# Optimization experiments

Measured on AMD Instinct MI355X. Metric: run time of the kernel, lower is better.

## Reference

```python
import jax, jax.numpy as jnp
import numpy as np

# Quantization / threshold constants (from init_kwargs)
AQI, AQF = 8, 8      # activation fixed-point: int/frac bits
NQI, NQF = 2, 8      # nonlinearity output fixed-point
TH_X = 0.1           # delta threshold on input
TH_H = 0.1           # delta threshold on hidden state


def _round_ste(x):
    # straight-through round (GradPreserveRoundTensor in the original util)
    return x + jax.lax.stop_gradient(jnp.round(x) - x)


def quantize(x, qi, qf):
    # util.quantize_tensor with quantize=1: fake-quantize to Q(qi).(qf) fixed point
    power = jnp.asarray(2.0 ** qf, x.dtype)
    clip_val = 2.0 ** (qi + qf - 1)
    return jnp.clip(_round_ste(x * power), -clip_val, clip_val - 1) / power


def setup_inputs() -> dict:
    key = jax.random.key(0)
    k0, k1, k2, k3, k4 = jax.random.split(key, 5)
    T, B, I, H = 512, 64, 512, 1024
    G = 4 * H
    return {
        "x": jax.random.normal(k0, (T, B, I), jnp.float32),
        "weight_ih": jax.random.normal(k1, (G, I), jnp.float32) / np.sqrt(I).astype(np.float32),
        "weight_hh": jax.random.normal(k2, (G, H), jnp.float32) / np.sqrt(H).astype(np.float32),
        "bias_ih": jax.random.normal(k3, (G,), jnp.float32) * 0.1,
        "bias_hh": jax.random.normal(k4, (G,), jnp.float32) * 0.1,
    }


def reference(x, weight_ih, weight_hh, bias_ih, bias_hh):
    T, B, I = x.shape
    H = weight_hh.shape[1]
    dt = x.dtype

    th_x_q = quantize(jnp.asarray(TH_X, dt), AQI, AQF)  # quantized threshold for delta mask
    th_h_q = quantize(jnp.asarray(TH_H, dt), AQI, AQF)

    xs = quantize(x, AQI, AQF)  # inputs quantized once up front

    # initial state (initialize_state with state=None)
    x_prev0 = jnp.zeros((B, I), dt)           # Q(zeros) == zeros
    h0 = jnp.zeros((B, H), dt)
    hp0 = jnp.zeros((B, H), dt)
    c0 = jnp.zeros((B, H), dt)
    m0 = jnp.zeros((B, 4 * H), dt) + bias_ih + bias_hh  # biases folded into m once
    reg0 = jnp.zeros((), dt)

    w_ih_t = weight_ih.T  # [I, 4H]
    w_hh_t = weight_hh.T  # [H, 4H]

    def step(carry, x_t):
        x_prev, h, h_prev, c, m, reg = carry
        dx = x_t - x_prev
        dh = h - h_prev
        dxa = jnp.abs(dx)
        dha = jnp.abs(dh)
        dx = jnp.where(dxa < th_x_q, jnp.asarray(0, dt), dx)   # masked_fill with quantized th
        dh = jnp.where(dha < th_h_q, jnp.asarray(0, dt), dh)
        x_prev = jnp.where(dxa >= TH_X, x_t, x_prev)           # state update with raw th (as in source)
        h_prev = jnp.where(dha >= TH_H, h, h_prev)
        reg = reg + jnp.sum(jnp.abs(dh))                       # l1 norm of masked delta_h

        m = dx @ w_ih_t + dh @ w_hh_t + m                      # delta-GEMM accumulated into m
        pre = quantize(m, AQI, AQF)
        p_i, p_f, p_g, p_o = jnp.split(pre, 4, axis=1)
        g_i = quantize(jax.nn.sigmoid(p_i), NQI, NQF)
        g_f = quantize(jax.nn.sigmoid(p_f), NQI, NQF)
        g_o = quantize(jax.nn.sigmoid(p_o), NQI, NQF)
        g_g = quantize(jnp.tanh(p_g), NQI, NQF)

        c_new = c * g_f + g_i * g_g
        q_c = quantize(c_new, AQI, AQF)
        c_tanh = quantize(jnp.tanh(q_c), NQI, NQF)
        h_new = quantize(g_o * c_tanh, AQI, AQF)
        return (x_prev, h_new, h_prev, q_c, m, reg), h_new

    (x_prev, h, h_prev, c, m, reg), out = jax.lax.scan(
        step, (x_prev0, h0, hp0, c0, m0, reg0), xs)

    # x_prev_out is padded to [B, max(I, H)] (zeros beyond input_size)
    x_prev_out = jnp.zeros((B, max(I, H)), dt).at[:, :I].set(x_prev)
    # state tensors stacked over layers (num_layers=1)
    state = (x_prev_out[None], h[None], h_prev[None], c[None], m[None])
    return (out, *state, reg.reshape(1))
```

## Files before the change

### kernel.cpp

```cpp
#include <hip/hip_runtime.h>
#include <hip/hip_fp16.h>
#include <stdint.h>

typedef unsigned short ushort_t;
typedef unsigned int uint_t;
typedef unsigned long long ull_t;
typedef _Float16 half8 __attribute__((ext_vector_type(8)));
typedef float f32x4 __attribute__((ext_vector_type(4)));

#define TSTEPS 512
#define BATCH  64
#define ISZ    512
#define HSZ    1024
#define GSZ    4096
#define NB     256
#define NTH    1024
#define DHFRAG 65536

static constexpr size_t OFF_XPREV = (size_t)TSTEPS * BATCH * HSZ;
static constexpr size_t OFF_H     = OFF_XPREV + (size_t)BATCH * 1024;
static constexpr size_t OFF_HP    = OFF_H  + (size_t)BATCH * HSZ;
static constexpr size_t OFF_C     = OFF_HP + (size_t)BATCH * HSZ;
static constexpr size_t OFF_M     = OFF_C  + (size_t)BATCH * HSZ;
static constexpr size_t OFF_REG   = OFF_M  + (size_t)BATCH * GSZ;

#define TH_RAW 0.1f
#define TH_QNT 0.1015625f

__device__ __forceinline__ float qA(float x) {
  float v = rintf(x * 256.0f);
  v = fminf(fmaxf(v, -32768.0f), 32767.0f);
  return v * 0.00390625f;
}
__device__ __forceinline__ float qN(float x) {
  float v = rintf(x * 256.0f);
  v = fminf(fmaxf(v, -512.0f), 511.0f);
  return v * 0.00390625f;
}
__device__ __forceinline__ float sigm(float x) { return 1.0f / (1.0f + expf(-x)); }

__global__ __launch_bounds__(256) void xscan_kernel(const float* __restrict__ x,
                                                    __half* __restrict__ dx16,
                                                    float* __restrict__ out_xprev) {
  const int gid = blockIdx.x * blockDim.x + threadIdx.x;
  float xp = 0.0f;
  #pragma unroll 8
  for (int t = 0; t < TSTEPS; t++) {
    float xq = qA(x[(size_t)t * (BATCH * ISZ) + gid]);
    float d  = xq - xp;
    float da = fabsf(d);
    dx16[(size_t)t * (BATCH * ISZ) + gid] = __float2half((da < TH_QNT) ? 0.0f : d);
    if (da >= TH_RAW) xp = xq;
  }
  const int b = gid >> 9;
  const int i = gid & 511;
  out_xprev[(size_t)b * 1024 + i]       = xp;
  out_xprev[(size_t)b * 1024 + 512 + i] = 0.0f;
}

__device__ __forceinline__ void gbar_arrive(int* flags, int e) {
  asm volatile("s_waitcnt vmcnt(0)" ::: "memory");
  __syncthreads();
  if (threadIdx.x == 0) {
    __hip_atomic_store(&flags[blockIdx.x], e, __ATOMIC_RELAXED, __HIP_MEMORY_SCOPE_AGENT);
  }
}
__device__ __forceinline__ void gbar_wait(int* flags, int e) {
  if (threadIdx.x < 64) {
    const ull_t* f64 = (const ull_t*)flags;
    const int l = threadIdx.x;
    bool done;
    do {
      ull_t a = __hip_atomic_load(f64 + l,      __ATOMIC_RELAXED, __HIP_MEMORY_SCOPE_AGENT);
      ull_t c = __hip_atomic_load(f64 + 64 + l, __ATOMIC_RELAXED, __HIP_MEMORY_SCOPE_AGENT);
      bool ok = ((int)a >= e) & ((int)(a >> 32) >= e) &
                ((int)c >= e) & ((int)(c >> 32) >= e);
      done = __all(ok);
      if (!done) __builtin_amdgcn_s_sleep(2);
    } while (!done);
  }
  __syncthreads();
}

__global__ __launch_bounds__(NTH, 4) void scan_kernel(
    const __half* __restrict__ dx16, const float* __restrict__ w_ih,
    const float* __restrict__ w_hh, const float* __restrict__ b_ih,
    const float* __restrict__ b_hh, float* __restrict__ out,
    __half* __restrict__ dh16, float* __restrict__ partials, int* flags) {
  __shared__ __align__(16) unsigned char dxbuf[2][65536];
  __shared__ float part[4][64][16];
  __shared__ float red[256];

  const int tid  = threadIdx.x;
  const int wid  = tid >> 6;
  const int lane = tid & 63;
  const int bt   = wid >> 2;
  const int kg   = wid & 3;
  const int lr   = lane & 15;
  const int lkb  = (lane >> 4) * 16;

  const int wrow = blockIdx.x * 4 + (lr & 3) + (lr >> 2) * HSZ;
  half8 wx[4], wh[8];
  #pragma unroll
  for (int kt = 0; kt < 4; ++kt) {
    const float* p = w_ih + (size_t)wrow * ISZ + kg * 128 + kt * 32 + (lane >> 4) * 8;
    half8 v;
    #pragma unroll
    for (int e = 0; e < 8; ++e) v[e] = (_Float16)p[e];
    wx[kt] = v;
  }
  #pragma unroll
  for (int kt = 0; kt < 8; ++kt) {
    const float* p = w_hh + (size_t)wrow * HSZ + kg * 256 + kt * 32 + (lane >> 4) * 8;
    half8 v;
    #pragma unroll
    for (int e = 0; e < 8; ++e) v[e] = (_Float16)p[e];
    wh[kt] = v;
  }

  const int jj = tid & 3;
  const int cb = tid >> 2;
  const int j  = blockIdx.x * 4 + jj;
  const int g0 = j, g1 = j + HSZ, g2 = j + 2 * HSZ, g3 = j + 3 * HSZ;
  float m0 = 0.f, m1 = 0.f, m2 = 0.f, m3 = 0.f;
  float c = 0.0f, hp = 0.0f, h = 0.0f, regacc = 0.0f;
  if (tid < 256) {
    m0 = b_ih[g0] + b_hh[g0];
    m1 = b_ih[g1] + b_hh[g1];
    m2 = b_ih[g2] + b_hh[g2];
    m3 = b_ih[g3] + b_hh[g3];
  }
  const size_t dhcell2 = ((size_t)(blockIdx.x >> 1) * 64 + cb) * 2 + (blockIdx.x & 1);

  const int arow = bt * 16 + lr;
  const int akey = (arow & 7) << 4;

  const int kc0 = kg * 32 + (lane >> 4);
  const int hrow = arow;

  {
    const ull_t* __restrict__ sx = (const ull_t*)dx16;
    #pragma unroll
    for (int i = 0; i < 8; ++i) {
      ull_t v = sx[i * 1024 + tid];
      const int u = i * 1024 + tid;
      const int row = u >> 7, cc = u & 127;
      *(ull_t*)(&dxbuf[0][0] + row * 1024 + ((cc * 8) ^ ((row & 7) << 4))) = v;
    }
  }
  __syncthreads();

  int epoch = 1;

  for (int t = 0; t < TSTEPS; t++) {
    const ull_t* __restrict__ hb = (const ull_t*)(dh16 + (size_t)(t & 1) * DHFRAG);
    const unsigned char* xbase = &dxbuf[t & 1][0] + arow * 1024;

    ull_t lo[4], hi[4];
    #pragma unroll
    for (int kt = 0; kt < 4; ++kt) {
      const size_t ci = ((size_t)(kc0 + kt * 4) * 64 + hrow) * 2;
      lo[kt] = __hip_atomic_load(hb + ci,     __ATOMIC_RELAXED, __HIP_MEMORY_SCOPE_AGENT);
      hi[kt] = __hip_atomic_load(hb + ci + 1, __ATOMIC_RELAXED, __HIP_MEMORY_SCOPE_AGENT);
    }

    f32x4 acc = {0.f, 0.f, 0.f, 0.f};
    {
      #pragma unroll
      for (int kt = 0; kt < 4; ++kt) {
        const int col = kg * 256 + kt * 64 + lkb;
        union { uint4 u; half8 hv; } U;
        U.u = *(const uint4*)(xbase + (col ^ akey));
        acc = __builtin_amdgcn_mfma_f32_16x16x32_f16(U.hv, wx[kt], acc, 0, 0, 0);
      }
    }

    ull_t lo2[4], hi2[4];
    #pragma unroll
    for (int kt = 0; kt < 4; ++kt) {
      const size_t ci = ((size_t)(kc0 + (kt + 4) * 4) * 64 + hrow) * 2;
      lo2[kt] = __hip_atomic_load(hb + ci,     __ATOMIC_RELAXED, __HIP_MEMORY_SCOPE_AGENT);
      hi2[kt] = __hip_atomic_load(hb + ci + 1, __ATOMIC_RELAXED, __HIP_MEMORY_SCOPE_AGENT);
    }
    #pragma unroll
    for (int kt = 0; kt < 4; ++kt) {
      union { ull_t u[2]; half8 hv; } U;
      U.u[0] = lo[kt]; U.u[1] = hi[kt];
      acc = __builtin_amdgcn_mfma_f32_16x16x32_f16(U.hv, wh[kt], acc, 0, 0, 0);
    }
    #pragma unroll
    for (int kt = 0; kt < 4; ++kt) {
      union { ull_t u[2]; half8 hv; } U;
      U.u[0] = lo2[kt]; U.u[1] = hi2[kt];
      acc = __builtin_amdgcn_mfma_f32_16x16x32_f16(U.hv, wh[kt + 4], acc, 0, 0, 0);
    }

    #pragma unroll
    for (int r = 0; r < 4; ++r)
      part[kg][bt * 16 + (lane >> 4) * 4 + r][lr] = acc[r];
    __syncthreads();

    if (tid < 256) {
      float s0 = 0.f, s1 = 0.f, s2 = 0.f, s3 = 0.f;
      #pragma unroll
      for (int k2 = 0; k2 < 4; ++k2) {
        s0 += part[k2][cb][jj];
        s1 += part[k2][cb][4 + jj];
        s2 += part[k2][cb][8 + jj];
        s3 += part[k2][cb][12 + jj];
      }
      m0 += s0; m1 += s1; m2 += s2; m3 += s3;

      float pi = qA(m0), pf = qA(m1), pg = qA(m2), po = qA(m3);
      float gi = qN(sigm(pi));
      float gf = qN(sigm(pf));
      float gg = qN(tanhf(pg));
      float go = qN(sigm(po));
      float cn = c * gf + gi * gg;
      c = qA(cn);
      float ct = qN(tanhf(c));
      h = qA(go * ct);
      out[(size_t)t * (BATCH * HSZ) + (size_t)cb * HSZ + j] = h;

      if (t < TSTEPS - 1) {
        float d  = h - hp;
        float da = fabsf(d);
        float dm = (da < TH_QNT) ? 0.0f : d;
        if (da >= TH_RAW) hp = h;
        regacc += fabsf(dm);
        ushort_t my = __half_as_ushort(__float2half(dm));
        int v1 = __shfl((int)my, lane + 1, 64);
        int v2 = __shfl((int)my, lane + 2, 64);
        int v3 = __shfl((int)my, lane + 3, 64);
        if (jj == 0) {
          ull_t dw = (ull_t)my | ((ull_t)(ushort_t)v1 << 16) |
                     ((ull_t)(ushort_t)v2 << 32) | ((ull_t)(ushort_t)v3 << 48);
          ull_t* dhw = (ull_t*)(dh16 + (size_t)((t + 1) & 1) * DHFRAG);
          __hip_atomic_store(dhw + dhcell2, dw,
                             __ATOMIC_RELAXED, __HIP_MEMORY_SCOPE_AGENT);
        }
      }
    }

    gbar_arrive(flags, epoch);

    if (t < TSTEPS - 1) {
      const ull_t* __restrict__ sx =
          (const ull_t*)(dx16 + (size_t)(t + 1) * (BATCH * ISZ));
      unsigned char* dst = &dxbuf[(t + 1) & 1][0];
      #pragma unroll
      for (int i = 0; i < 8; ++i) {
        ull_t v = sx[i * 1024 + tid];
        const int u = i * 1024 + tid;
        const int row = u >> 7, cc = u & 127;
        *(ull_t*)(dst + row * 1024 + ((cc * 8) ^ ((row & 7) << 4))) = v;
      }
    }

    gbar_wait(flags, epoch);
    epoch++;
  }

  if (tid < 256) {
    out[OFF_H  + (size_t)cb * HSZ + j] = h;
    out[OFF_HP + (size_t)cb * HSZ + j] = hp;
    out[OFF_C  + (size_t)cb * HSZ + j] = c;
    out[OFF_M  + (size_t)cb * GSZ + g0] = m0;
    out[OFF_M  + (size_t)cb * GSZ + g1] = m1;
    out[OFF_M  + (size_t)cb * GSZ + g2] = m2;
    out[OFF_M  + (size_t)cb * GSZ + g3] = m3;
  }

  if (tid < 256) red[tid] = regacc;
  __syncthreads();
  for (int s = 128; s > 0; s >>= 1) {
    if (tid < s) red[tid] += red[tid + s];
    __syncthreads();
  }
  if (tid == 0)
    __hip_atomic_store(&partials[blockIdx.x], red[0], __ATOMIC_RELAXED, __HIP_MEMORY_SCOPE_AGENT);
  gbar_arrive(flags, epoch);
  gbar_wait(flags, epoch);
  epoch++;
  if (blockIdx.x == 0) {
    if (tid < 256)
      red[tid] = __hip_atomic_load(&partials[tid], __ATOMIC_RELAXED, __HIP_MEMORY_SCOPE_AGENT);
    __syncthreads();
    for (int s = 128; s > 0; s >>= 1) {
      if (tid < s) red[tid] += red[tid + s];
      __syncthreads();
    }
    if (tid == 0) out[OFF_REG] = red[0];
  }
}

extern "C" void kernel_launch(void* const* d_in, const int* in_sizes, int n_in,
                              void* d_out, int out_size, void* d_ws, size_t ws_size,
                              hipStream_t stream) {
  const float* x    = (const float*)d_in[0];
  const float* w_ih = (const float*)d_in[1];
  const float* w_hh = (const float*)d_in[2];
  const float* b_ih = (const float*)d_in[3];
  const float* b_hh = (const float*)d_in[4];
  float* out = (float*)d_out;

  const size_t dx_elems = (size_t)TSTEPS * BATCH * ISZ;
  __half* dx16     = (__half*)d_ws;
  __half* dh16     = dx16 + dx_elems;
  float*  partials = (float*)(dh16 + 2 * (size_t)DHFRAG);
  int*    flags    = (int*)(partials + NB);
  size_t needed = (size_t)((char*)(flags + NB) - (char*)d_ws);
  if (ws_size < needed) return;

  (void)hipMemsetAsync(dh16, 0, 2 * (size_t)DHFRAG * sizeof(__half), stream);
  (void)hipMemsetAsync(flags, 0, NB * sizeof(int), stream);
  xscan_kernel<<<128, 256, 0, stream>>>(x, dx16, out + OFF_XPREV);
  scan_kernel<<<NB, NTH, 0, stream>>>(dx16, w_ih, w_hh, b_ih, b_hh, out,
                                      dh16, partials, flags);
}
```

Baseline: 2.660 ms.

## Split batch into two groups with separate grid barriers to pipeline recurrent steps

Each timestep's batch of 64 is split into two groups of 32, each with its own dh buffer and flag set. Each block processes one group, arrives on that group's barrier, and only then waits on the other group's barrier, so barrier latency for one group can overlap compute for the other. The K dimension is split across 8 wave groups instead of 4, with a padded partial-sum buffer to cut LDS bank conflicts. Blocks are remapped to a permuted hidden-unit index. This adds a barrier and a __syncthreads per group, and the gbar_wait/arrive helpers are now called with the timestep as the epoch, so correctness depends on those helpers matching that convention.

```diff
diff --git a/kernel.cpp b/kernel.cpp
--- a/kernel.cpp
+++ b/kernel.cpp
@@ -15,7 +15,7 @@
 #define GSZ    4096
 #define NB     256
 #define NTH    1024
-#define DHFRAG 65536
+#define DHG    32768
 
 static constexpr size_t OFF_XPREV = (size_t)TSTEPS * BATCH * HSZ;
 static constexpr size_t OFF_H     = OFF_XPREV + (size_t)BATCH * 1024;
@@ -86,41 +86,45 @@
     const __half* __restrict__ dx16, const float* __restrict__ w_ih,
     const float* __restrict__ w_hh, const float* __restrict__ b_ih,
     const float* __restrict__ b_hh, float* __restrict__ out,
-    __half* __restrict__ dh16, float* __restrict__ partials, int* flags) {
+    __half* __restrict__ dhf, float* __restrict__ partials,
+    int* flags0, int* flags1) {
   __shared__ __align__(16) unsigned char dxbuf[2][65536];
-  __shared__ float part[4][64][16];
+  __shared__ float part[8][32][17];
   __shared__ float red[256];
 
   const int tid  = threadIdx.x;
   const int wid  = tid >> 6;
   const int lane = tid & 63;
-  const int bt   = wid >> 2;
-  const int kg   = wid & 3;
+  const int bt   = wid >> 3;
+  const int kgi  = wid & 7;
   const int lr   = lane & 15;
-  const int lkb  = (lane >> 4) * 16;
-
-  const int wrow = blockIdx.x * 4 + (lr & 3) + (lr >> 2) * HSZ;
-  half8 wx[4], wh[8];
+  const int lq   = lane >> 4;
+  const int lkb  = lq * 16;
+  const int jb   = (blockIdx.x & 7) * 32 + (blockIdx.x >> 3);
+
+  const int wrow = jb * 4 + (lr & 3) + (lr >> 2) * HSZ;
+  half8 wx[2], wh[4];
   #pragma unroll
-  for (int kt = 0; kt < 4; ++kt) {
-    const float* p = w_ih + (size_t)wrow * ISZ + kg * 128 + kt * 32 + (lane >> 4) * 8;
+  for (int kt = 0; kt < 2; ++kt) {
+    const float* p = w_ih + (size_t)wrow * ISZ + kgi * 64 + kt * 32 + lq * 8;
     half8 v;
     #pragma unroll
     for (int e = 0; e < 8; ++e) v[e] = (_Float16)p[e];
     wx[kt] = v;
   }
   #pragma unroll
-  for (int kt = 0; kt < 8; ++kt) {
-    const float* p = w_hh + (size_t)wrow * HSZ + kg * 256 + kt * 32 + (lane >> 4) * 8;
+  for (int kt = 0; kt < 4; ++kt) {
+    const float* p = w_hh + (size_t)wrow * HSZ + kgi * 128 + kt * 32 + lq * 8;
     half8 v;
     #pragma unroll
     for (int e = 0; e < 8; ++e) v[e] = (_Float16)p[e];
     wh[kt] = v;
   }
 
+  const int g_me = tid >> 7;
   const int jj = tid & 3;
-  const int cb = tid >> 2;
-  const int j  = blockIdx.x * 4 + jj;
+  const int bl = (tid >> 2) & 31;
+  const int j  = jb * 4 + jj;
   const int g0 = j, g1 = j + HSZ, g2 = j + 2 * HSZ, g3 = j + 3 * HSZ;
   float m0 = 0.f, m1 = 0.f, m2 = 0.f, m3 = 0.f;
   float c = 0.0f, hp = 0.0f, h = 0.0f, regacc = 0.0f;
@@ -130,13 +134,10 @@
     m2 = b_ih[g2] + b_hh[g2];
     m3 = b_ih[g3] + b_hh[g3];
   }
-  const size_t dhcell2 = ((size_t)(blockIdx.x >> 1) * 64 + cb) * 2 + (blockIdx.x & 1);
+  const size_t dhcell2 = ((size_t)(jb >> 1) * 32 + bl) * 2 + (jb & 1);
 
   const int arow = bt * 16 + lr;
   const int akey = (arow & 7) << 4;
-
-  const int kc0 = kg * 32 + (lane >> 4);
-  const int hrow = arow;
 
   {
     const ull_t* __restrict__ sx = (const ull_t*)dx16;
@@ -150,125 +151,112 @@
   }
   __syncthreads();
 
-  int epoch = 1;
-
   for (int t = 0; t < TSTEPS; t++) {
-    const ull_t* __restrict__ hb = (const ull_t*)(dh16 + (size_t)(t & 1) * DHFRAG);
-    const unsigned char* xbase = &dxbuf[t & 1][0] + arow * 1024;
-
-    ull_t lo[4], hi[4];
     #pragma unroll
-    for (int kt = 0; kt < 4; ++kt) {
-      const size_t ci = ((size_t)(kc0 + kt * 4) * 64 + hrow) * 2;
-      lo[kt] = __hip_atomic_load(hb + ci,     __ATOMIC_RELAXED, __HIP_MEMORY_SCOPE_AGENT);
-      hi[kt] = __hip_atomic_load(hb + ci + 1, __ATOMIC_RELAXED, __HIP_MEMORY_SCOPE_AGENT);
-    }
-
-    f32x4 acc = {0.f, 0.f, 0.f, 0.f};
-    {
+    for (int g = 0; g < 2; ++g) {
+      gbar_wait(g == 0 ? flags0 : flags1, t);
+
+      const ull_t* __restrict__ hb =
+          (const ull_t*)(dhf + (size_t)(g * 2 + (t & 1)) * DHG);
+      ull_t lo[4], hi[4];
       #pragma unroll
       for (int kt = 0; kt < 4; ++kt) {
-        const int col = kg * 256 + kt * 64 + lkb;
-        union { uint4 u; half8 hv; } U;
-        U.u = *(const uint4*)(xbase + (col ^ akey));
-        acc = __builtin_amdgcn_mfma_f32_16x16x32_f16(U.hv, wx[kt], acc, 0, 0, 0);
+        const size_t ci = ((size_t)(kgi * 16 + kt * 4 + lq) * 32 + arow) * 2;
+        lo[kt] = __hip_atomic_load(hb + ci,     __ATOMIC_RELAXED, __HIP_MEMORY_SCOPE_AGENT);
+        hi[kt] = __hip_atomic_load(hb + ci + 1, __ATOMIC_RELAXED, __HIP_MEMORY_SCOPE_AGENT);
+      }
+
+      f32x4 acc = {0.f, 0.f, 0.f, 0.f};
+      {
+        const unsigned char* xbase = &dxbuf[t & 1][0] + (g * 32 + arow) * 1024;
+        #pragma unroll
+        for (int kt = 0; kt < 2; ++kt) {
+          const int col = kgi * 128 + kt * 64 + lkb;
+          union { uint4 u; half8 hv; } U;
+          U.u = *(const uint4*)(xbase + (col ^ akey));
+          acc = __builtin_amdgcn_mfma_f32_16x16x32_f16(U.hv, wx[kt], acc, 0, 0, 0);
+        }
+      }
+      #pragma unroll
+      for (int kt = 0; kt < 4; ++kt) {
+        union { ull_t u[2]; half8 hv; } U;
+        U.u[0] = lo[kt]; U.u[1] = hi[kt];
+        acc = __builtin_amdgcn_mfma_f32_16x16x32_f16(U.hv, wh[kt], acc, 0, 0, 0);
+      }
+
+      #pragma unroll
+      for (int r = 0; r < 4; ++r)
+        part[kgi][bt * 16 + lq * 4 + r][lr] = acc[r];
+      __syncthreads();
+
+      if (tid < 256 && g_me == g) {
+        float s0 = 0.f, s1 = 0.f, s2 = 0.f, s3 = 0.f;
+        #pragma unroll
+        for (int k2 = 0; k2 < 8; ++k2) {
+          s0 += part[k2][bl][jj];
+          s1 += part[k2][bl][4 + jj];
+          s2 += part[k2][bl][8 + jj];
+          s3 += part[k2][bl][12 + jj];
+        }
+        m0 += s0; m1 += s1; m2 += s2; m3 += s3;
+
+        float pi = qA(m0), pf = qA(m1), pg = qA(m2), po = qA(m3);
+        float gi = qN(sigm(pi));
+        float gf = qN(sigm(pf));
+        float gg = qN(tanhf(pg));
+        float go = qN(sigm(po));
+        float cn = c * gf + gi * gg;
+        c = qA(cn);
+        float ct = qN(tanhf(c));
+        h = qA(go * ct);
+        out[(size_t)t * (BATCH * HSZ) + (size_t)(g * 32 + bl) * HSZ + j] = h;
+
+        if (t < TSTEPS - 1) {
+          float d  = h - hp;
+          float da = fabsf(d);
+          float dm = (da < TH_QNT) ? 0.0f : d;
+          if (da >= TH_RAW) hp = h;
+          regacc += fabsf(dm);
+          ushort_t my = __half_as_ushort(__float2half(dm));
+          int v1 = __shfl((int)my, lane + 1, 64);
+          int v2 = __shfl((int)my, lane + 2, 64);
+          int v3 = __shfl((int)my, lane + 3, 64);
+          if (jj == 0) {
+            ull_t dw = (ull_t)my | ((ull_t)(ushort_t)v1 << 16) |
+                       ((ull_t)(ushort_t)v2 << 32) | ((ull_t)(ushort_t)v3 << 48);
+            ull_t* dhw = (ull_t*)(dhf + (size_t)(g * 2 + ((t + 1) & 1)) * DHG);
+            __hip_atomic_store(dhw + dhcell2, dw,
+                               __ATOMIC_RELAXED, __HIP_MEMORY_SCOPE_AGENT);
+          }
+        }
+      }
+
+      gbar_arrive(g == 0 ? flags0 : flags1, t + 1);
+
+      if (g == 0 && t + 1 < TSTEPS) {
+        const ull_t* __restrict__ sx =
+            (const ull_t*)(dx16 + (size_t)(t + 1) * (BATCH * ISZ));
+        unsigned char* dst = &dxbuf[(t + 1) & 1][0];
+        #pragma unroll
+        for (int i = 0; i < 8; ++i) {
+          ull_t v = sx[i * 1024 + tid];
+          const int u = i * 1024 + tid;
+          const int row = u >> 7, cc = u & 127;
+          *(ull_t*)(dst + row * 1024 + ((cc * 8) ^ ((row & 7) << 4))) = v;
+        }
       }
     }
-
-    ull_t lo2[4], hi2[4];
-    #pragma unroll
-    for (int kt = 0; kt < 4; ++kt) {
-      const size_t ci = ((size_t)(kc0 + (kt + 4) * 4) * 64 + hrow) * 2;
-      lo2[kt] = __hip_atomic_load(hb + ci,     __ATOMIC_RELAXED, __HIP_MEMORY_SCOPE_AGENT);
-      hi2[kt] = __hip_atomic_load(hb + ci + 1, __ATOMIC_RELAXED, __HIP_MEMORY_SCOPE_AGENT);
-    }
-    #pragma unroll
-    for (int kt = 0; kt < 4; ++kt) {
-      union { ull_t u[2]; half8 hv; } U;
-      U.u[0] = lo[kt]; U.u[1] = hi[kt];
-      acc = __builtin_amdgcn_mfma_f32_16x16x32_f16(U.hv, wh[kt], acc, 0, 0, 0);
-    }
-    #pragma unroll
-    for (int kt = 0; kt < 4; ++kt) {
-      union { ull_t u[2]; half8 hv; } U;
-      U.u[0] = lo2[kt]; U.u[1] = hi2[kt];
-      acc = __builtin_amdgcn_mfma_f32_16x16x32_f16(U.hv, wh[kt + 4], acc, 0, 0, 0);
-    }
-
-    #pragma unroll
-    for (int r = 0; r < 4; ++r)
-      part[kg][bt * 16 + (lane >> 4) * 4 + r][lr] = acc[r];
-    __syncthreads();
-
-    if (tid < 256) {
-      float s0 = 0.f, s1 = 0.f, s2 = 0.f, s3 = 0.f;
-      #pragma unroll
-      for (int k2 = 0; k2 < 4; ++k2) {
-        s0 += part[k2][cb][jj];
-        s1 += part[k2][cb][4 + jj];
-        s2 += part[k2][cb][8 + jj];
-        s3 += part[k2][cb][12 + jj];
-      }
-      m0 += s0; m1 += s1; m2 += s2; m3 += s3;
-
-      float pi = qA(m0), pf = qA(m1), pg = qA(m2), po = qA(m3);
-      float gi = qN(sigm(pi));
-      float gf = qN(sigm(pf));
-      float gg = qN(tanhf(pg));
-      float go = qN(sigm(po));
-      float cn = c * gf + gi * gg;
-      c = qA(cn);
-      float ct = qN(tanhf(c));
-      h = qA(go * ct);
-      out[(size_t)t * (BATCH * HSZ) + (size_t)cb * HSZ + j] = h;
-
-      if (t < TSTEPS - 1) {
-        float d  = h - hp;
-        float da = fabsf(d);
-        float dm = (da < TH_QNT) ? 0.0f : d;
-        if (da >= TH_RAW) hp = h;
-        regacc += fabsf(dm);
-        ushort_t my = __half_as_ushort(__float2half(dm));
-        int v1 = __shfl((int)my, lane + 1, 64);
-        int v2 = __shfl((int)my, lane + 2, 64);
-        int v3 = __shfl((int)my, lane + 3, 64);
-        if (jj == 0) {
-          ull_t dw = (ull_t)my | ((ull_t)(ushort_t)v1 << 16) |
-                     ((ull_t)(ushort_t)v2 << 32) | ((ull_t)(ushort_t)v3 << 48);
-          ull_t* dhw = (ull_t*)(dh16 + (size_t)((t + 1) & 1) * DHFRAG);
-          __hip_atomic_store(dhw + dhcell2, dw,
-                             __ATOMIC_RELAXED, __HIP_MEMORY_SCOPE_AGENT);
-        }
-      }
-    }
-
-    gbar_arrive(flags, epoch);
-
-    if (t < TSTEPS - 1) {
-      const ull_t* __restrict__ sx =
-          (const ull_t*)(dx16 + (size_t)(t + 1) * (BATCH * ISZ));
-      unsigned char* dst = &dxbuf[(t + 1) & 1][0];
-      #pragma unroll
-      for (int i = 0; i < 8; ++i) {
-        ull_t v = sx[i * 1024 + tid];
-        const int u = i * 1024 + tid;
-        const int row = u >> 7, cc = u & 127;
-        *(ull_t*)(dst + row * 1024 + ((cc * 8) ^ ((row & 7) << 4))) = v;
-      }
-    }
-
-    gbar_wait(flags, epoch);
-    epoch++;
   }
 
   if (tid < 256) {
-    out[OFF_H  + (size_t)cb * HSZ + j] = h;
-    out[OFF_HP + (size_t)cb * HSZ + j] = hp;
-    out[OFF_C  + (size_t)cb * HSZ + j] = c;
-    out[OFF_M  + (size_t)cb * GSZ + g0] = m0;
-    out[OFF_M  + (size_t)cb * GSZ + g1] = m1;
-    out[OFF_M  + (size_t)cb * GSZ + g2] = m2;
-    out[OFF_M  + (size_t)cb * GSZ + g3] = m3;
+    const int b = g_me * 32 + bl;
+    out[OFF_H  + (size_t)b * HSZ + j] = h;
+    out[OFF_HP + (size_t)b * HSZ + j] = hp;
+    out[OFF_C  + (size_t)b * HSZ + j] = c;
+    out[OFF_M  + (size_t)b * GSZ + g0] = m0;
+    out[OFF_M  + (size_t)b * GSZ + g1] = m1;
+    out[OFF_M  + (size_t)b * GSZ + g2] = m2;
+    out[OFF_M  + (size_t)b * GSZ + g3] = m3;
   }
 
   if (tid < 256) red[tid] = regacc;
@@ -279,9 +267,8 @@
   }
   if (tid == 0)
     __hip_atomic_store(&partials[blockIdx.x], red[0], __ATOMIC_RELAXED, __HIP_MEMORY_SCOPE_AGENT);
-  gbar_arrive(flags, epoch);
-  gbar_wait(flags, epoch);
-  epoch++;
+  gbar_arrive(flags0, TSTEPS + 1);
+  gbar_wait(flags0, TSTEPS + 1);
   if (blockIdx.x == 0) {
     if (tid < 256)
       red[tid] = __hip_atomic_load(&partials[tid], __ATOMIC_RELAXED, __HIP_MEMORY_SCOPE_AGENT);
@@ -306,15 +293,16 @@
 
   const size_t dx_elems = (size_t)TSTEPS * BATCH * ISZ;
   __half* dx16     = (__half*)d_ws;
-  __half* dh16     = dx16 + dx_elems;
-  float*  partials = (float*)(dh16 + 2 * (size_t)DHFRAG);
-  int*    flags    = (int*)(partials + NB);
-  size_t needed = (size_t)((char*)(flags + NB) - (char*)d_ws);
+  __half* dhf      = dx16 + dx_elems;
+  float*  partials = (float*)(dhf + 4 * (size_t)DHG);
+  int*    flags0   = (int*)(partials + NB);
+  int*    flags1   = flags0 + NB;
+  size_t needed = (size_t)((char*)(flags1 + NB) - (char*)d_ws);
   if (ws_size < needed) return;
 
-  (void)hipMemsetAsync(dh16, 0, 2 * (size_t)DHFRAG * sizeof(__half), stream);
-  (void)hipMemsetAsync(flags, 0, NB * sizeof(int), stream);
+  (void)hipMemsetAsync(dhf, 0, 4 * (size_t)DHG * sizeof(__half), stream);
+  (void)hipMemsetAsync(flags0, 0, 2 * NB * sizeof(int), stream);
   xscan_kernel<<<128, 256, 0, stream>>>(x, dx16, out + OFF_XPREV);
   scan_kernel<<<NB, NTH, 0, stream>>>(dx16, w_ih, w_hh, b_ih, b_hh, out,
-                                      dh16, partials, flags);
-}
+                                      dhf, partials, flags0, flags1);
+}
```

After: 3.758 ms. +41.2%, slower.

## Move input-projection MFMA and output store off the grid-barrier critical path

Applied to the files above, without the earlier changes.

Restructures the persistent scan loop so the input-projection MFMAs for step t+1 and the h output store run after the barrier arrive, overlapping the wait. The barrier wait now sits at the top of each step. It also remaps blocks to hidden-column groups with a strided permutation and pads the shared partial-sum array to 17 columns to reduce bank conflicts. This adds an extra __syncthreads per step and changes barrier epoch numbering.

```diff
diff --git a/kernel.cpp b/kernel.cpp
--- a/kernel.cpp
+++ b/kernel.cpp
@@ -88,7 +88,7 @@
     const float* __restrict__ b_hh, float* __restrict__ out,
     __half* __restrict__ dh16, float* __restrict__ partials, int* flags) {
   __shared__ __align__(16) unsigned char dxbuf[2][65536];
-  __shared__ float part[4][64][16];
+  __shared__ float part[4][64][17];
   __shared__ float red[256];
 
   const int tid  = threadIdx.x;
@@ -97,13 +97,15 @@
   const int bt   = wid >> 2;
   const int kg   = wid & 3;
   const int lr   = lane & 15;
-  const int lkb  = (lane >> 4) * 16;
-
-  const int wrow = blockIdx.x * 4 + (lr & 3) + (lr >> 2) * HSZ;
+  const int lq   = lane >> 4;
+  const int lkb  = lq * 16;
+  const int jb   = (blockIdx.x & 7) * 32 + (blockIdx.x >> 3);
+
+  const int wrow = jb * 4 + (lr & 3) + (lr >> 2) * HSZ;
   half8 wx[4], wh[8];
   #pragma unroll
   for (int kt = 0; kt < 4; ++kt) {
-    const float* p = w_ih + (size_t)wrow * ISZ + kg * 128 + kt * 32 + (lane >> 4) * 8;
+    const float* p = w_ih + (size_t)wrow * ISZ + kg * 128 + kt * 32 + lq * 8;
     half8 v;
     #pragma unroll
     for (int e = 0; e < 8; ++e) v[e] = (_Float16)p[e];
@@ -111,7 +113,7 @@
   }
   #pragma unroll
   for (int kt = 0; kt < 8; ++kt) {
-    const float* p = w_hh + (size_t)wrow * HSZ + kg * 256 + kt * 32 + (lane >> 4) * 8;
+    const float* p = w_hh + (size_t)wrow * HSZ + kg * 256 + kt * 32 + lq * 8;
     half8 v;
     #pragma unroll
     for (int e = 0; e < 8; ++e) v[e] = (_Float16)p[e];
@@ -120,7 +122,7 @@
 
   const int jj = tid & 3;
   const int cb = tid >> 2;
-  const int j  = blockIdx.x * 4 + jj;
+  const int j  = jb * 4 + jj;
   const int g0 = j, g1 = j + HSZ, g2 = j + 2 * HSZ, g3 = j + 3 * HSZ;
   float m0 = 0.f, m1 = 0.f, m2 = 0.f, m3 = 0.f;
   float c = 0.0f, hp = 0.0f, h = 0.0f, regacc = 0.0f;
@@ -130,13 +132,11 @@
     m2 = b_ih[g2] + b_hh[g2];
     m3 = b_ih[g3] + b_hh[g3];
   }
-  const size_t dhcell2 = ((size_t)(blockIdx.x >> 1) * 64 + cb) * 2 + (blockIdx.x & 1);
+  const size_t dhcell2 = ((size_t)(jb >> 1) * 64 + cb) * 2 + (jb & 1);
 
   const int arow = bt * 16 + lr;
   const int akey = (arow & 7) << 4;
-
-  const int kc0 = kg * 32 + (lane >> 4);
-  const int hrow = arow;
+  const int kc0  = kg * 32 + lq;
 
   {
     const ull_t* __restrict__ sx = (const ull_t*)dx16;
@@ -150,54 +150,39 @@
   }
   __syncthreads();
 
-  int epoch = 1;
+  f32x4 acc = {0.f, 0.f, 0.f, 0.f};
+  {
+    const unsigned char* xbase = &dxbuf[0][0] + arow * 1024;
+    #pragma unroll
+    for (int kt = 0; kt < 4; ++kt) {
+      const int col = kg * 256 + kt * 64 + lkb;
+      union { uint4 u; half8 hv; } U;
+      U.u = *(const uint4*)(xbase + (col ^ akey));
+      acc = __builtin_amdgcn_mfma_f32_16x16x32_f16(U.hv, wx[kt], acc, 0, 0, 0);
+    }
+  }
 
   for (int t = 0; t < TSTEPS; t++) {
+    gbar_wait(flags, t);
+
     const ull_t* __restrict__ hb = (const ull_t*)(dh16 + (size_t)(t & 1) * DHFRAG);
-    const unsigned char* xbase = &dxbuf[t & 1][0] + arow * 1024;
-
-    ull_t lo[4], hi[4];
-    #pragma unroll
-    for (int kt = 0; kt < 4; ++kt) {
-      const size_t ci = ((size_t)(kc0 + kt * 4) * 64 + hrow) * 2;
+    ull_t lo[8], hi[8];
+    #pragma unroll
+    for (int kt = 0; kt < 8; ++kt) {
+      const size_t ci = ((size_t)(kc0 + kt * 4) * 64 + arow) * 2;
       lo[kt] = __hip_atomic_load(hb + ci,     __ATOMIC_RELAXED, __HIP_MEMORY_SCOPE_AGENT);
       hi[kt] = __hip_atomic_load(hb + ci + 1, __ATOMIC_RELAXED, __HIP_MEMORY_SCOPE_AGENT);
     }
-
-    f32x4 acc = {0.f, 0.f, 0.f, 0.f};
-    {
-      #pragma unroll
-      for (int kt = 0; kt < 4; ++kt) {
-        const int col = kg * 256 + kt * 64 + lkb;
-        union { uint4 u; half8 hv; } U;
-        U.u = *(const uint4*)(xbase + (col ^ akey));
-        acc = __builtin_amdgcn_mfma_f32_16x16x32_f16(U.hv, wx[kt], acc, 0, 0, 0);
-      }
-    }
-
-    ull_t lo2[4], hi2[4];
-    #pragma unroll
-    for (int kt = 0; kt < 4; ++kt) {
-      const size_t ci = ((size_t)(kc0 + (kt + 4) * 4) * 64 + hrow) * 2;
-      lo2[kt] = __hip_atomic_load(hb + ci,     __ATOMIC_RELAXED, __HIP_MEMORY_SCOPE_AGENT);
-      hi2[kt] = __hip_atomic_load(hb + ci + 1, __ATOMIC_RELAXED, __HIP_MEMORY_SCOPE_AGENT);
-    }
-    #pragma unroll
-    for (int kt = 0; kt < 4; ++kt) {
+    #pragma unroll
+    for (int kt = 0; kt < 8; ++kt) {
       union { ull_t u[2]; half8 hv; } U;
       U.u[0] = lo[kt]; U.u[1] = hi[kt];
       acc = __builtin_amdgcn_mfma_f32_16x16x32_f16(U.hv, wh[kt], acc, 0, 0, 0);
     }
-    #pragma unroll
-    for (int kt = 0; kt < 4; ++kt) {
-      union { ull_t u[2]; half8 hv; } U;
-      U.u[0] = lo2[kt]; U.u[1] = hi2[kt];
-      acc = __builtin_amdgcn_mfma_f32_16x16x32_f16(U.hv, wh[kt + 4], acc, 0, 0, 0);
-    }
 
     #pragma unroll
     for (int r = 0; r < 4; ++r)
-      part[kg][bt * 16 + (lane >> 4) * 4 + r][lr] = acc[r];
+      part[kg][bt * 16 + lq * 4 + r][lr] = acc[r];
     __syncthreads();
 
     if (tid < 256) {
@@ -220,7 +205,6 @@
       c = qA(cn);
       float ct = qN(tanhf(c));
       h = qA(go * ct);
-      out[(size_t)t * (BATCH * HSZ) + (size_t)cb * HSZ + j] = h;
 
       if (t < TSTEPS - 1) {
         float d  = h - hp;
@@ -242,23 +226,37 @@
       }
     }
 
-    gbar_arrive(flags, epoch);
-
-    if (t < TSTEPS - 1) {
-      const ull_t* __restrict__ sx =
-          (const ull_t*)(dx16 + (size_t)(t + 1) * (BATCH * ISZ));
-      unsigned char* dst = &dxbuf[(t + 1) & 1][0];
-      #pragma unroll
-      for (int i = 0; i < 8; ++i) {
-        ull_t v = sx[i * 1024 + tid];
-        const int u = i * 1024 + tid;
-        const int row = u >> 7, cc = u & 127;
-        *(ull_t*)(dst + row * 1024 + ((cc * 8) ^ ((row & 7) << 4))) = v;
+    gbar_arrive(flags, t + 1);
+
+    if (tid < 256)
+      out[(size_t)t * (BATCH * HSZ) + (size_t)cb * HSZ + j] = h;
+
+    if (t + 1 < TSTEPS) {
+      {
+        const ull_t* __restrict__ sx =
+            (const ull_t*)(dx16 + (size_t)(t + 1) * (BATCH * ISZ));
+        unsigned char* dst = &dxbuf[(t + 1) & 1][0];
+        #pragma unroll
+        for (int i = 0; i < 8; ++i) {
+          ull_t v = sx[i * 1024 + tid];
+          const int u = i * 1024 + tid;
+          const int row = u >> 7, cc = u & 127;
+          *(ull_t*)(dst + row * 1024 + ((cc * 8) ^ ((row & 7) << 4))) = v;
+        }
       }
-    }
-
-    gbar_wait(flags, epoch);
-    epoch++;
+      __syncthreads();
+      {
+        acc = (f32x4){0.f, 0.f, 0.f, 0.f};
+        const unsigned char* xbase = &dxbuf[(t + 1) & 1][0] + arow * 1024;
+        #pragma unroll
+        for (int kt = 0; kt < 4; ++kt) {
+          const int col = kg * 256 + kt * 64 + lkb;
+          union { uint4 u; half8 hv; } U;
+          U.u = *(const uint4*)(xbase + (col ^ akey));
+          acc = __builtin_amdgcn_mfma_f32_16x16x32_f16(U.hv, wx[kt], acc, 0, 0, 0);
+        }
+      }
+    }
   }
 
   if (tid < 256) {
@@ -279,9 +277,8 @@
   }
   if (tid == 0)
     __hip_atomic_store(&partials[blockIdx.x], red[0], __ATOMIC_RELAXED, __HIP_MEMORY_SCOPE_AGENT);
-  gbar_arrive(flags, epoch);
-  gbar_wait(flags, epoch);
-  epoch++;
+  gbar_arrive(flags, TSTEPS + 1);
+  gbar_wait(flags, TSTEPS + 1);
   if (blockIdx.x == 0) {
     if (tid < 256)
       red[tid] = __hip_atomic_load(&partials[tid], __ATOMIC_RELAXED, __HIP_MEMORY_SCOPE_AGENT);
```

Result: slower. 2.898 ms (+8.9%).
